# Performance work log

Hardware: AMD Instinct MI355X
Metric: run time of the kernel (lower is better)

The kernel has to match this reference:

```python
import jax, jax.numpy as jnp
import numpy as np

N = 100000
E = 1600000
F_IN = 64
HID = 64
OUT = 64


def _sage_conv(x, src, dst, w_l, b_l, w_r):
    # PyG SAGEConv (mean aggr): out = lin_l(mean_{j in N(i)} x_j) + lin_r(x_i)
    msgs = x[src]                                             # [E, F] gather
    summed = jax.ops.segment_sum(msgs, dst, num_segments=N)   # [N, F]
    ones = jnp.ones((src.shape[0],), dtype=x.dtype)
    cnt = jax.ops.segment_sum(ones, dst, num_segments=N)      # [N]
    mean = summed / jnp.maximum(cnt, 1.0)[:, None]
    return mean @ w_l + b_l + x @ w_r


def setup_inputs() -> dict:
    key = jax.random.key(0)
    ks = jax.random.split(key, 12)
    sc = lambda f: 1.0 / np.sqrt(f)
    inp = {
        "h": jax.random.normal(ks[0], (N, F_IN), dtype=jnp.float32),
        "edge_index": jax.random.randint(ks[1], (2, E), 0, N, dtype=jnp.int64),
        # conv1: lin_l (with bias) and lin_r (no bias), weights stored [in, out]
        "w1_l": jax.random.normal(ks[2], (F_IN, HID), dtype=jnp.float32) * sc(F_IN),
        "b1_l": jnp.zeros((HID,), dtype=jnp.float32),
        "w1_r": jax.random.normal(ks[3], (F_IN, HID), dtype=jnp.float32) * sc(F_IN),
        "w_lin1": jax.random.normal(ks[4], (HID, HID), dtype=jnp.float32) * sc(HID),
        "b_lin1": jnp.zeros((HID,), dtype=jnp.float32),
        "w2_l": jax.random.normal(ks[5], (HID, HID), dtype=jnp.float32) * sc(HID),
        "b2_l": jnp.zeros((HID,), dtype=jnp.float32),
        "w2_r": jax.random.normal(ks[6], (HID, HID), dtype=jnp.float32) * sc(HID),
        "w_lin2": jax.random.normal(ks[7], (HID, OUT), dtype=jnp.float32) * sc(HID),
        "b_lin2": jnp.zeros((OUT,), dtype=jnp.float32),
    }
    return inp


def reference(h, edge_index, w1_l, b1_l, w1_r, w_lin1, b_lin1,
              w2_l, b2_l, w2_r, w_lin2, b_lin2):
    src, dst = edge_index[0], edge_index[1]
    x = jax.nn.relu(_sage_conv(h, src, dst, w1_l, b1_l, w1_r))
    x = jax.nn.relu(x @ w_lin1 + b_lin1)
    x = jax.nn.relu(_sage_conv(x, src, dst, w2_l, b2_l, w2_r))
    x = x @ w_lin2 + b_lin2
    return x
```

## Files before the change

### kernel.cpp

```cpp
#include <hip/hip_runtime.h>
#include <hip/hip_fp16.h>

#define FEAT   64
#define BSHIFT 8
#define BNODES 256
#define MAXB   512
#define CHUNK  4096
#define REGION 5120

typedef _Float16 half8 __attribute__((ext_vector_type(8)));
typedef float  float4v __attribute__((ext_vector_type(4)));

__global__ __launch_bounds__(256) void setup_kernel(
    const float* __restrict__ h, __half* __restrict__ h16, int n4, int CB,
    const float* w0, const float* w1, const float* w2,
    const float* w3, const float* w4, const float* w5,
    __half* __restrict__ wT, int* __restrict__ bcur)
{
    int b = blockIdx.x;
    if (b < CB) {
        int i = b * 256 + threadIdx.x;
        if (i < n4) {
            float4 v = ((const float4*)h)[i];
            union { uint2 u; __half2 h2[2]; } r;
            r.h2[0] = __floats2half2_rn(v.x, v.y);
            r.h2[1] = __floats2half2_rn(v.z, v.w);
            ((uint2*)h16)[i] = r.u;
        }
    } else if (b < CB + 96) {
        int bb = b - CB;
        int m = bb >> 4;
        int idx = ((bb & 15) << 8) | threadIdx.x;
        const float* src = m==0?w0 : m==1?w1 : m==2?w2 : m==3?w3 : m==4?w4 : w5;
        int o = idx >> 6, i = idx & 63;
        wT[m * 4096 + o * 64 + i] = __float2half(src[i * 64 + o]);
    } else {
        bcur[threadIdx.x] = 0;
        bcur[threadIdx.x + 256] = 0;
    }
}

__global__ __launch_bounds__(512) void partition_kernel(
    const int* __restrict__ src, const int* __restrict__ dst,
    int* __restrict__ bcur, int* __restrict__ pedge, int E)
{
    __shared__ int cnt[MAXB];
    __shared__ int sa[MAXB], sb[MAXB];
    __shared__ int gb[MAXB];
    __shared__ int lcur[MAXB];
    __shared__ int stage[CHUNK];
    __shared__ int tgt[CHUNK];

    int tid = threadIdx.x;
    cnt[tid] = 0;
    __syncthreads();

    int base = blockIdx.x * CHUNK;
    int vals[8];
    int bs[8];
#pragma unroll
    for (int i = 0; i < 8; i++) {
        int e = base + tid + i * 512;
        bs[i] = -1;
        if (e < E) {
            int s_ = src[e];
            int d_ = dst[e];
            int b  = d_ >> BSHIFT;
            bs[i]  = b;
            vals[i] = s_ | ((d_ & (BNODES - 1)) << 20);
            atomicAdd(&cnt[b], 1);
        }
    }
    __syncthreads();

    sa[tid] = cnt[tid];
    __syncthreads();
    int* cur = sa; int* nxt = sb;
    for (int off = 1; off < MAXB; off <<= 1) {
        nxt[tid] = cur[tid] + ((tid >= off) ? cur[tid - off] : 0);
        __syncthreads();
        int* tmp = cur; cur = nxt; nxt = tmp;
    }
    {
        int c = cnt[tid];
        int lo = cur[tid] - c;
        int gbase = c ? atomicAdd(&bcur[tid], c) : 0;
        if (gbase > REGION) gbase = REGION;
        gb[tid]   = tid * REGION + gbase - lo;
        lcur[tid] = lo;
    }
    __syncthreads();

#pragma unroll
    for (int i = 0; i < 8; i++) {
        if (bs[i] >= 0) {
            int pos = atomicAdd(&lcur[bs[i]], 1);
            stage[pos] = vals[i];
            tgt[pos]   = gb[bs[i]];
        }
    }
    __syncthreads();

    int cn = min(CHUNK, E - base);
    for (int i = tid; i < cn; i += 512)
        pedge[tgt[i] + i] = stage[i];
}

__global__ __launch_bounds__(512) void buildcsr_kernel(
    const int* __restrict__ pedge, const int* __restrict__ bcur,
    unsigned* __restrict__ rowinfo, int* __restrict__ csr, int N)
{
    __shared__ int stg[REGION];
    __shared__ int srt[REGION];
    __shared__ int hist[BNODES], scn[BNODES], lcur[BNODES];
    int b = blockIdx.x;
    int tid = threadIdx.x;
    int beg = b * REGION;
    int cnt = min(bcur[b], REGION);

    if (tid < BNODES) hist[tid] = 0;
    __syncthreads();

    for (int i = tid; i < cnt; i += 512) {
        int p = pedge[beg + i];
        stg[i] = p;
        atomicAdd(&hist[p >> 20], 1);
    }
    __syncthreads();

    int v = 0;
    if (tid < BNODES) { v = hist[tid]; scn[tid] = v; }
    __syncthreads();
    for (int off = 1; off < BNODES; off <<= 1) {
        int t = 0;
        if (tid < BNODES && tid >= off) t = scn[tid - off];
        __syncthreads();
        if (tid < BNODES) scn[tid] += t;
        __syncthreads();
    }
    if (tid < BNODES) {
        int excl = scn[tid] - v;
        int node = (b << BSHIFT) + tid;
        if (node < N)
            rowinfo[node] = (unsigned)(beg + excl) | ((unsigned)v << 21);
        lcur[tid] = excl;
    }
    __syncthreads();

    for (int i = tid; i < cnt; i += 512) {
        int p = stg[i];
        int pos = atomicAdd(&lcur[p >> 20], 1);
        srt[pos] = p & 0xFFFFF;
    }
    __syncthreads();
    for (int i = tid; i < cnt; i += 512)
        csr[beg + i] = srt[i];
}

__global__ __launch_bounds__(256) void gather_kernel(
    const __half* __restrict__ x, const unsigned* __restrict__ rowinfo,
    const int* __restrict__ csr_src, __half* __restrict__ mean, int N)
{
    int node = blockIdx.x * 4 + (threadIdx.x >> 6);
    if (node >= N) return;
    int lane = threadIdx.x & 63;
    int g  = lane >> 3;
    int s8 = lane & 7;
    unsigned info = rowinfo[node];
    int beg = (int)(info & 0x1FFFFFu);
    int deg = (int)(info >> 21);
    int end = beg + deg;

    float acc[8] = {0.f,0.f,0.f,0.f,0.f,0.f,0.f,0.f};
    int e = beg + g;
    for (; e + 8 < end; e += 16) {
        int i0 = csr_src[e];
        int i1 = csr_src[e + 8];
        union { uint4 u; __half2 h2[4]; } r0, r1;
        r0.u = ((const uint4*)(x + (size_t)i0 * FEAT))[s8];
        r1.u = ((const uint4*)(x + (size_t)i1 * FEAT))[s8];
#pragma unroll
        for (int t = 0; t < 4; t++) {
            float2 f0 = __half22float2(r0.h2[t]);
            float2 f1 = __half22float2(r1.h2[t]);
            acc[2*t]   += f0.x + f1.x;
            acc[2*t+1] += f0.y + f1.y;
        }
    }
    if (e < end) {
        int i0 = csr_src[e];
        union { uint4 u; __half2 h2[4]; } r0;
        r0.u = ((const uint4*)(x + (size_t)i0 * FEAT))[s8];
#pragma unroll
        for (int t = 0; t < 4; t++) {
            float2 f0 = __half22float2(r0.h2[t]);
            acc[2*t]   += f0.x;
            acc[2*t+1] += f0.y;
        }
    }
#pragma unroll
    for (int mask = 8; mask <= 32; mask <<= 1)
#pragma unroll
        for (int t = 0; t < 8; t++)
            acc[t] += __shfl_xor(acc[t], mask, 64);
    if (g == 0) {
        float inv = deg ? 1.0f / (float)deg : 0.0f;
        union { uint4 u; __half2 h2[4]; } o;
        o.h2[0] = __floats2half2_rn(acc[0]*inv, acc[1]*inv);
        o.h2[1] = __floats2half2_rn(acc[2]*inv, acc[3]*inv);
        o.h2[2] = __floats2half2_rn(acc[4]*inv, acc[5]*inv);
        o.h2[3] = __floats2half2_rn(acc[6]*inv, acc[7]*inv);
        ((uint4*)(mean + (size_t)node * FEAT))[s8] = o.u;
    }
}

__global__ __launch_bounds__(256) void node_mfma_kernel(
    const __half* __restrict__ mean16, const __half* __restrict__ self16,
    const __half* __restrict__ wlT, const __half* __restrict__ wrT,
    const __half* __restrict__ w2T,
    const float* __restrict__ b1, const float* __restrict__ b2,
    float* __restrict__ out_f, __half* __restrict__ out_h,
    int n, int relu_out)
{
    __shared__ _Float16 s1[64][68];
    int wave = threadIdx.x >> 6;
    int lane = threadIdx.x & 63;
    int r = lane & 15;
    int q = lane >> 4;
    int base = blockIdx.x * 64 + wave * 16;

    int arow = min(base + r, n - 1);
    const half8* mrow = (const half8*)(mean16 + (size_t)arow * FEAT);
    const half8* xrow = (const half8*)(self16 + (size_t)arow * FEAT);
    half8 Am0 = mrow[q], Am1 = mrow[4 + q];
    half8 Ax0 = xrow[q], Ax1 = xrow[4 + q];

    float4v acc[4];
#pragma unroll
    for (int c = 0; c < 4; c++) {
        float bv = b1[c * 16 + r];
        acc[c] = (float4v){bv, bv, bv, bv};
        const half8* bl = (const half8*)(wlT + (size_t)(c * 16 + r) * FEAT);
        const half8* br = (const half8*)(wrT + (size_t)(c * 16 + r) * FEAT);
        acc[c] = __builtin_amdgcn_mfma_f32_16x16x32_f16(Am0, bl[q],     acc[c], 0, 0, 0);
        acc[c] = __builtin_amdgcn_mfma_f32_16x16x32_f16(Am1, bl[4 + q], acc[c], 0, 0, 0);
        acc[c] = __builtin_amdgcn_mfma_f32_16x16x32_f16(Ax0, br[q],     acc[c], 0, 0, 0);
        acc[c] = __builtin_amdgcn_mfma_f32_16x16x32_f16(Ax1, br[4 + q], acc[c], 0, 0, 0);
    }
#pragma unroll
    for (int c = 0; c < 4; c++)
#pragma unroll
        for (int t = 0; t < 4; t++)
            s1[wave * 16 + q * 4 + t][c * 16 + r] = (_Float16)fmaxf(acc[c][t], 0.0f);
    __syncthreads();

    union { uint2 u2[2]; half8 h; } A2[2];
#pragma unroll
    for (int s = 0; s < 2; s++) {
        const _Float16* p = &s1[wave * 16 + r][s * 32 + q * 8];
        A2[s].u2[0] = *(const uint2*)p;
        A2[s].u2[1] = *(const uint2*)(p + 4);
    }

    float4v acc2[4];
#pragma unroll
    for (int c = 0; c < 4; c++) {
        float bv = b2[c * 16 + r];
        acc2[c] = (float4v){bv, bv, bv, bv};
        const half8* bw = (const half8*)(w2T + (size_t)(c * 16 + r) * FEAT);
        acc2[c] = __builtin_amdgcn_mfma_f32_16x16x32_f16(A2[0].h, bw[q],     acc2[c], 0, 0, 0);
        acc2[c] = __builtin_amdgcn_mfma_f32_16x16x32_f16(A2[1].h, bw[4 + q], acc2[c], 0, 0, 0);
    }

#pragma unroll
    for (int c = 0; c < 4; c++)
#pragma unroll
        for (int t = 0; t < 4; t++) {
            int gr = base + q * 4 + t;
            if (gr < n) {
                float v = acc2[c][t];
                if (relu_out) v = fmaxf(v, 0.0f);
                if (out_h) out_h[(size_t)gr * FEAT + c * 16 + r] = __float2half(v);
                else       out_f[(size_t)gr * FEAT + c * 16 + r] = v;
            }
        }
}

extern "C" void kernel_launch(void* const* d_in, const int* in_sizes, int n_in,
                              void* d_out, int out_size, void* d_ws, size_t ws_size,
                              hipStream_t stream) {
    const float* h      = (const float*)d_in[0];
    const int*   ei     = (const int*)d_in[1];
    const float* w1_l   = (const float*)d_in[2];
    const float* b1_l   = (const float*)d_in[3];
    const float* w1_r   = (const float*)d_in[4];
    const float* w_lin1 = (const float*)d_in[5];
    const float* b_lin1 = (const float*)d_in[6];
    const float* w2_l   = (const float*)d_in[7];
    const float* b2_l   = (const float*)d_in[8];
    const float* w2_r   = (const float*)d_in[9];
    const float* w_lin2 = (const float*)d_in[10];
    const float* b_lin2 = (const float*)d_in[11];

    const int N = in_sizes[0] / FEAT;
    const int E = in_sizes[1] / 2;
    const int* src  = ei;
    const int* dst_ = ei + E;

    const int NB = (N + BNODES - 1) >> BSHIFT;
    const int PB = (E + CHUNK - 1) / CHUNK;
    const int n4 = N * FEAT / 4;
    const int CB = (n4 + 255) / 256;
    const int tblk = (N + 63) / 64;
    const int gblk = (N + 3) / 4;

    size_t off = 0;
    int* bcur       = (int*)d_ws + off; off += MAXB;
    unsigned* rowinfo = (unsigned*)((int*)d_ws + off); off += (size_t)N;
    off = (off + 3) & ~(size_t)3;
    int* csr    = (int*)d_ws + off; off += (size_t)NB * REGION + 64;
    off = (off + 3) & ~(size_t)3;
    __half* h16 = (__half*)((int*)d_ws + off); off += (size_t)N * FEAT / 2;
    __half* x2h = (__half*)((int*)d_ws + off); off += (size_t)N * FEAT / 2;
    __half* wT  = (__half*)((int*)d_ws + off); off += 6 * 2048;
    __half* mean16 = (__half*)((int*)d_ws + off); off += (size_t)N * FEAT / 2;
    int* pedge  = (int*)mean16;

    setup_kernel<<<CB + 96 + 1, 256, 0, stream>>>(
        h, h16, n4, CB, w1_l, w1_r, w_lin1, w2_l, w2_r, w_lin2, wT, bcur);
    partition_kernel<<<PB, 512, 0, stream>>>(src, dst_, bcur, pedge, E);
    buildcsr_kernel<<<NB, 512, 0, stream>>>(pedge, bcur, rowinfo, csr, N);

    gather_kernel<<<gblk, 256, 0, stream>>>(h16, rowinfo, csr, mean16, N);
    node_mfma_kernel<<<tblk, 256, 0, stream>>>(mean16, h16,
                                               wT + 0 * 4096, wT + 1 * 4096, wT + 2 * 4096,
                                               b1_l, b_lin1,
                                               (float*)nullptr, x2h, N, 1);

    gather_kernel<<<gblk, 256, 0, stream>>>(x2h, rowinfo, csr, mean16, N);
    node_mfma_kernel<<<tblk, 256, 0, stream>>>(mean16, x2h,
                                               wT + 3 * 4096, wT + 4 * 4096, wT + 5 * 4096,
                                               b2_l, b_lin2,
                                               (float*)d_out, (__half*)nullptr, N, 0);
}
```

Measured before the change: 251.9 us.

## Fuse neighbor-mean gather into the per-layer MFMA node kernel via shared memory

Merges the gather kernel and the node MFMA kernel into one per-layer kernel. Each 64-node block computes the neighbor means into shared memory and then feeds them straight into the MFMA transforms, so the fp16 mean buffer no longer makes a global round trip and two launches are removed. The gather mapping changes from one wave with 8 edge groups per node to 16 threads with 2 edge groups per node, processing 4 nodes sequentially. This lowers per-node memory-level parallelism and can add load imbalance within a block. The partition staging buffer now gets its own workspace region instead of aliasing the mean buffer.

```diff
diff --git a/kernel.cpp b/kernel.cpp
--- a/kernel.cpp
+++ b/kernel.cpp
@@ -157,110 +157,113 @@
         csr[beg + i] = srt[i];
 }
 
-__global__ __launch_bounds__(256) void gather_kernel(
+__global__ __launch_bounds__(256) void fused_layer_kernel(
     const __half* __restrict__ x, const unsigned* __restrict__ rowinfo,
-    const int* __restrict__ csr_src, __half* __restrict__ mean, int N)
-{
-    int node = blockIdx.x * 4 + (threadIdx.x >> 6);
-    if (node >= N) return;
-    int lane = threadIdx.x & 63;
-    int g  = lane >> 3;
-    int s8 = lane & 7;
-    unsigned info = rowinfo[node];
-    int beg = (int)(info & 0x1FFFFFu);
-    int deg = (int)(info >> 21);
-    int end = beg + deg;
-
-    float acc[8] = {0.f,0.f,0.f,0.f,0.f,0.f,0.f,0.f};
-    int e = beg + g;
-    for (; e + 8 < end; e += 16) {
-        int i0 = csr_src[e];
-        int i1 = csr_src[e + 8];
-        union { uint4 u; __half2 h2[4]; } r0, r1;
-        r0.u = ((const uint4*)(x + (size_t)i0 * FEAT))[s8];
-        r1.u = ((const uint4*)(x + (size_t)i1 * FEAT))[s8];
-#pragma unroll
-        for (int t = 0; t < 4; t++) {
-            float2 f0 = __half22float2(r0.h2[t]);
-            float2 f1 = __half22float2(r1.h2[t]);
-            acc[2*t]   += f0.x + f1.x;
-            acc[2*t+1] += f0.y + f1.y;
-        }
-    }
-    if (e < end) {
-        int i0 = csr_src[e];
-        union { uint4 u; __half2 h2[4]; } r0;
-        r0.u = ((const uint4*)(x + (size_t)i0 * FEAT))[s8];
-#pragma unroll
-        for (int t = 0; t < 4; t++) {
-            float2 f0 = __half22float2(r0.h2[t]);
-            acc[2*t]   += f0.x;
-            acc[2*t+1] += f0.y;
-        }
-    }
-#pragma unroll
-    for (int mask = 8; mask <= 32; mask <<= 1)
-#pragma unroll
-        for (int t = 0; t < 8; t++)
-            acc[t] += __shfl_xor(acc[t], mask, 64);
-    if (g == 0) {
-        float inv = deg ? 1.0f / (float)deg : 0.0f;
-        union { uint4 u; __half2 h2[4]; } o;
-        o.h2[0] = __floats2half2_rn(acc[0]*inv, acc[1]*inv);
-        o.h2[1] = __floats2half2_rn(acc[2]*inv, acc[3]*inv);
-        o.h2[2] = __floats2half2_rn(acc[4]*inv, acc[5]*inv);
-        o.h2[3] = __floats2half2_rn(acc[6]*inv, acc[7]*inv);
-        ((uint4*)(mean + (size_t)node * FEAT))[s8] = o.u;
-    }
-}
-
-__global__ __launch_bounds__(256) void node_mfma_kernel(
-    const __half* __restrict__ mean16, const __half* __restrict__ self16,
+    const int* __restrict__ csr_src,
     const __half* __restrict__ wlT, const __half* __restrict__ wrT,
     const __half* __restrict__ w2T,
     const float* __restrict__ b1, const float* __restrict__ b2,
     float* __restrict__ out_f, __half* __restrict__ out_h,
     int n, int relu_out)
 {
-    __shared__ _Float16 s1[64][68];
-    int wave = threadIdx.x >> 6;
-    int lane = threadIdx.x & 63;
-    int r = lane & 15;
-    int q = lane >> 4;
+    __shared__ __attribute__((aligned(16))) _Float16 sbuf[64][72];
+
+    int tid  = threadIdx.x;
+    int wave = tid >> 6;
+    int lane = tid & 63;
+    int sg   = tid >> 4;
+    int gg   = (tid >> 3) & 1;
+    int s8   = tid & 7;
+    int r    = lane & 15;
+    int q    = lane >> 4;
     int base = blockIdx.x * 64 + wave * 16;
 
     int arow = min(base + r, n - 1);
-    const half8* mrow = (const half8*)(mean16 + (size_t)arow * FEAT);
-    const half8* xrow = (const half8*)(self16 + (size_t)arow * FEAT);
-    half8 Am0 = mrow[q], Am1 = mrow[4 + q];
+    const half8* xrow = (const half8*)(x + (size_t)arow * FEAT);
     half8 Ax0 = xrow[q], Ax1 = xrow[4 + q];
 
-    float4v acc[4];
+    unsigned infos[4];
+#pragma unroll
+    for (int i = 0; i < 4; i++) {
+        int node = blockIdx.x * 64 + sg * 4 + i;
+        infos[i] = (node < n) ? rowinfo[node] : 0u;
+    }
+
+#pragma unroll
+    for (int i = 0; i < 4; i++) {
+        int beg = (int)(infos[i] & 0x1FFFFFu);
+        int deg = (int)(infos[i] >> 21);
+        int end = beg + deg;
+        float acc[8] = {0.f,0.f,0.f,0.f,0.f,0.f,0.f,0.f};
+        int e = beg + gg;
+        for (; e + 2 < end; e += 4) {
+            int i0 = csr_src[e];
+            int i1 = csr_src[e + 2];
+            union { uint4 u; __half2 h2[4]; } r0, r1;
+            r0.u = ((const uint4*)(x + (size_t)i0 * FEAT))[s8];
+            r1.u = ((const uint4*)(x + (size_t)i1 * FEAT))[s8];
+#pragma unroll
+            for (int t = 0; t < 4; t++) {
+                float2 f0 = __half22float2(r0.h2[t]);
+                float2 f1 = __half22float2(r1.h2[t]);
+                acc[2*t]   += f0.x + f1.x;
+                acc[2*t+1] += f0.y + f1.y;
+            }
+        }
+        if (e < end) {
+            int i0 = csr_src[e];
+            union { uint4 u; __half2 h2[4]; } r0;
+            r0.u = ((const uint4*)(x + (size_t)i0 * FEAT))[s8];
+#pragma unroll
+            for (int t = 0; t < 4; t++) {
+                float2 f0 = __half22float2(r0.h2[t]);
+                acc[2*t]   += f0.x;
+                acc[2*t+1] += f0.y;
+            }
+        }
+#pragma unroll
+        for (int t = 0; t < 8; t++)
+            acc[t] += __shfl_xor(acc[t], 8, 64);
+        if (gg == 0) {
+            float inv = deg ? 1.0f / (float)deg : 0.0f;
+            union { uint4 u; __half2 h2[4]; } o;
+            o.h2[0] = __floats2half2_rn(acc[0]*inv, acc[1]*inv);
+            o.h2[1] = __floats2half2_rn(acc[2]*inv, acc[3]*inv);
+            o.h2[2] = __floats2half2_rn(acc[4]*inv, acc[5]*inv);
+            o.h2[3] = __floats2half2_rn(acc[6]*inv, acc[7]*inv);
+            int ln = sg * 4 + i;
+            *(uint4*)&sbuf[ln][s8 * 8] = o.u;
+        }
+    }
+    __syncthreads();
+
+    union { uint4 u4; half8 h; } Am0u, Am1u;
+    Am0u.u4 = *(const uint4*)&sbuf[wave * 16 + r][q * 8];
+    Am1u.u4 = *(const uint4*)&sbuf[wave * 16 + r][(4 + q) * 8];
+
+    float4v acc1[4];
 #pragma unroll
     for (int c = 0; c < 4; c++) {
         float bv = b1[c * 16 + r];
-        acc[c] = (float4v){bv, bv, bv, bv};
+        acc1[c] = (float4v){bv, bv, bv, bv};
         const half8* bl = (const half8*)(wlT + (size_t)(c * 16 + r) * FEAT);
         const half8* br = (const half8*)(wrT + (size_t)(c * 16 + r) * FEAT);
-        acc[c] = __builtin_amdgcn_mfma_f32_16x16x32_f16(Am0, bl[q],     acc[c], 0, 0, 0);
-        acc[c] = __builtin_amdgcn_mfma_f32_16x16x32_f16(Am1, bl[4 + q], acc[c], 0, 0, 0);
-        acc[c] = __builtin_amdgcn_mfma_f32_16x16x32_f16(Ax0, br[q],     acc[c], 0, 0, 0);
-        acc[c] = __builtin_amdgcn_mfma_f32_16x16x32_f16(Ax1, br[4 + q], acc[c], 0, 0, 0);
+        acc1[c] = __builtin_amdgcn_mfma_f32_16x16x32_f16(Am0u.h, bl[q],     acc1[c], 0, 0, 0);
+        acc1[c] = __builtin_amdgcn_mfma_f32_16x16x32_f16(Am1u.h, bl[4 + q], acc1[c], 0, 0, 0);
+        acc1[c] = __builtin_amdgcn_mfma_f32_16x16x32_f16(Ax0,    br[q],     acc1[c], 0, 0, 0);
+        acc1[c] = __builtin_amdgcn_mfma_f32_16x16x32_f16(Ax1,    br[4 + q], acc1[c], 0, 0, 0);
     }
 #pragma unroll
     for (int c = 0; c < 4; c++)
 #pragma unroll
         for (int t = 0; t < 4; t++)
-            s1[wave * 16 + q * 4 + t][c * 16 + r] = (_Float16)fmaxf(acc[c][t], 0.0f);
-    __syncthreads();
-
-    union { uint2 u2[2]; half8 h; } A2[2];
-#pragma unroll
-    for (int s = 0; s < 2; s++) {
-        const _Float16* p = &s1[wave * 16 + r][s * 32 + q * 8];
-        A2[s].u2[0] = *(const uint2*)p;
-        A2[s].u2[1] = *(const uint2*)(p + 4);
-    }
+            sbuf[wave * 16 + q * 4 + t][c * 16 + r] = (_Float16)fmaxf(acc1[c][t], 0.0f);
+    __syncthreads();
+
+    union { uint4 u4; half8 h; } A2[2];
+#pragma unroll
+    for (int s = 0; s < 2; s++)
+        A2[s].u4 = *(const uint4*)&sbuf[wave * 16 + r][s * 32 + q * 8];
 
     float4v acc2[4];
 #pragma unroll
@@ -311,8 +314,7 @@
     const int PB = (E + CHUNK - 1) / CHUNK;
     const int n4 = N * FEAT / 4;
     const int CB = (n4 + 255) / 256;
-    const int tblk = (N + 63) / 64;
-    const int gblk = (N + 3) / 4;
+    const int fblk = (N + 63) / 64;
 
     size_t off = 0;
     int* bcur       = (int*)d_ws + off; off += MAXB;
@@ -323,23 +325,20 @@
     __half* h16 = (__half*)((int*)d_ws + off); off += (size_t)N * FEAT / 2;
     __half* x2h = (__half*)((int*)d_ws + off); off += (size_t)N * FEAT / 2;
     __half* wT  = (__half*)((int*)d_ws + off); off += 6 * 2048;
-    __half* mean16 = (__half*)((int*)d_ws + off); off += (size_t)N * FEAT / 2;
-    int* pedge  = (int*)mean16;
+    int* pedge  = (int*)d_ws + off; off += (size_t)NB * REGION;
 
     setup_kernel<<<CB + 96 + 1, 256, 0, stream>>>(
         h, h16, n4, CB, w1_l, w1_r, w_lin1, w2_l, w2_r, w_lin2, wT, bcur);
     partition_kernel<<<PB, 512, 0, stream>>>(src, dst_, bcur, pedge, E);
     buildcsr_kernel<<<NB, 512, 0, stream>>>(pedge, bcur, rowinfo, csr, N);
 
-    gather_kernel<<<gblk, 256, 0, stream>>>(h16, rowinfo, csr, mean16, N);
-    node_mfma_kernel<<<tblk, 256, 0, stream>>>(mean16, h16,
-                                               wT + 0 * 4096, wT + 1 * 4096, wT + 2 * 4096,
-                                               b1_l, b_lin1,
-                                               (float*)nullptr, x2h, N, 1);
-
-    gather_kernel<<<gblk, 256, 0, stream>>>(x2h, rowinfo, csr, mean16, N);
-    node_mfma_kernel<<<tblk, 256, 0, stream>>>(mean16, x2h,
-                                               wT + 3 * 4096, wT + 4 * 4096, wT + 5 * 4096,
-                                               b2_l, b_lin2,
-                                               (float*)d_out, (__half*)nullptr, N, 0);
-}
+    fused_layer_kernel<<<fblk, 256, 0, stream>>>(
+        h16, rowinfo, csr,
+        wT + 0 * 4096, wT + 1 * 4096, wT + 2 * 4096,
+        b1_l, b_lin1, (float*)nullptr, x2h, N, 1);
+
+    fused_layer_kernel<<<fblk, 256, 0, stream>>>(
+        x2h, rowinfo, csr,
+        wT + 3 * 4096, wT + 4 * 4096, wT + 5 * 4096,
+        b2_l, b_lin2, (float*)d_out, (__half*)nullptr, N, 0);
+}
```

Measured after the change: 249.7 us. No clear change (-0.9%).
